# Optimization experiments

Measured on AMD Instinct MI355X. Metric: run time of the kernel, lower is better.

## Reference

```python
import jax, jax.numpy as jnp
import numpy as np

B, G, C = 8, 512, 32  # batch, grid size, channel width (INIT_DIM)
NPB = 32768           # nonzeros per batch element


def _sconv(x, k, stride, pad):
    # dense conv; sparse semantics recovered by masking with the output
    # coordinate occupancy (Minkowski conv only produces active outputs)
    return jax.lax.conv_general_dilated(
        x, k, (stride, stride), [(pad, pad), (pad, pad)],
        dimension_numbers=('NHWC', 'HWIO', 'NHWC'))


def _downsample_mask(m):
    # ME strided output coord exists iff any input coord in the 2x2 cell is active
    return jax.lax.reduce_window(m, 0.0, jax.lax.max, (1, 2, 2, 1), (1, 2, 2, 1), 'VALID')


def setup_inputs() -> dict:
    key = jax.random.key(0)
    ks = jax.random.split(key, 16)
    b = jnp.repeat(jnp.arange(B, dtype=jnp.int32), NPB)
    yx = jax.random.randint(ks[0], (B * NPB, 2), 0, G, dtype=jnp.int32)
    coords = jnp.concatenate([b[:, None], yx], axis=1)          # [N,3] (b,y,x)
    feats = jax.random.normal(ks[1], (B * NPB, 1), jnp.float32)  # 1 feature/nnz
    x2 = jax.random.normal(ks[2], (B, 3), jnp.float32)
    # Minkowski conv kernels (bias=False by default); HWIO layout
    K1 = jax.random.normal(ks[3], (5, 5, 1, C), jnp.float32) * 0.28   # kaiming-ish
    K2 = jax.random.normal(ks[4], (3, 3, C, C), jnp.float32) * 0.083
    K3 = jax.random.normal(ks[5], (3, 3, C, C), jnp.float32) * 0.083
    K4 = jax.random.normal(ks[6], (3, 3, C, C), jnp.float32) * 0.083
    # feature MLP: Linear(3,64) -> ReLU -> Linear(64,32)
    W1 = jax.random.normal(ks[7], (3, 64), jnp.float32) * 0.3
    b1 = jnp.zeros((64,), jnp.float32)
    W2 = jax.random.normal(ks[8], (64, 32), jnp.float32) * 0.25
    b2 = jnp.zeros((32,), jnp.float32)
    # matrix_embedding: Linear(64,128) -> ReLU
    W3 = jax.random.normal(ks[9], (64, 128), jnp.float32) * 0.18
    b3 = jnp.zeros((128,), jnp.float32)
    return {'coords': coords, 'feats': feats, 'x2': x2,
            'K1': K1, 'K2': K2, 'K3': K3, 'K4': K4,
            'W1': W1, 'b1': b1, 'W2': W2, 'b2': b2, 'W3': W3, 'b3': b3}


def reference(coords, feats, x2, K1, K2, K3, K4, W1, b1, W2, b2, W3, b3):
    bi, yi, xi = coords[:, 0], coords[:, 1], coords[:, 2]
    grid = jnp.zeros((B, G, G, 1), jnp.float32).at[bi, yi, xi, 0].set(feats[:, 0])
    m1 = jnp.zeros((B, G, G, 1), jnp.float32).at[bi, yi, xi, 0].set(1.0)
    # layer1: k=5 s=1 (output coords == input coords)
    y1 = jax.nn.relu(_sconv(grid, K1, 1, 2)) * m1
    # layers 2-4: k=3 s=2; centered at even positions, masked by strided occupancy
    m2 = _downsample_mask(m1)
    y2 = jax.nn.relu(_sconv(y1, K2, 2, 1)) * m2
    m3 = _downsample_mask(m2)
    y3 = jax.nn.relu(_sconv(y2, K3, 2, 1)) * m3
    m4 = _downsample_mask(m3)
    y4 = jax.nn.relu(_sconv(y3, K4, 2, 1)) * m4
    # global average pool over active output coordinates per batch
    cnt = jnp.sum(m4, axis=(1, 2))                      # [B,1]
    pooled = jnp.sum(y4, axis=(1, 2)) / jnp.maximum(cnt, 1.0)  # [B,32]
    # aux feature MLP
    h = jax.nn.relu(x2[:, :3] @ W1 + b1) @ W2 + b2      # [B,32]
    z = jnp.concatenate([pooled, h], axis=1)            # [B,64]
    return jax.nn.relu(z @ W3 + b3)                     # [B,128]
```

## Files before the change

### kernel.cpp

```cpp
#include <hip/hip_runtime.h>
#include <hip/hip_bf16.h>
#include <stdint.h>


static constexpr int G_ = 512;
static constexpr int NPTS = 8 * 32768;

#define DEVI __device__ __forceinline__

typedef __attribute__((ext_vector_type(8))) short bf16x8;
typedef __attribute__((ext_vector_type(4))) float f32x4;

DEVI float bf_lo(unsigned w) { return __uint_as_float(w << 16); }
DEVI float bf_hi(unsigned w) { return __uint_as_float(w & 0xFFFF0000u); }
DEVI unsigned comp(const uint4& v, int i) {
  return i == 0 ? v.x : i == 1 ? v.y : i == 2 ? v.z : v.w;
}
DEVI unsigned short f2bf_bits(float f) {
  unsigned u = __float_as_uint(f);
  unsigned r = u + 0x7FFFu + ((u >> 16) & 1u);
  return (unsigned short)(r >> 16);
}

__global__ __launch_bounds__(256) void k_scatter(const int* __restrict__ coords,
                                                 int* __restrict__ idxg) {
  int i = blockIdx.x * 256 + threadIdx.x;
  if (i >= NPTS) return;
  int b = coords[3 * i], y = coords[3 * i + 1], x = coords[3 * i + 2];
  atomicMax(&idxg[((size_t)b * G_ + y) * G_ + x], i);
}

__global__ __launch_bounds__(256) void k_grid(const int* __restrict__ idxg,
                                              const float* __restrict__ feats,
                                              float* __restrict__ grid) {
  int i = blockIdx.x * 256 + threadIdx.x;
  int v = idxg[i];
  grid[i] = (v >= 0) ? feats[v] : 0.0f;
}

__global__ __launch_bounds__(256) void k_m2(const int* __restrict__ idxg,
                                            float* __restrict__ m2) {
  int i = blockIdx.x * 256 + threadIdx.x;
  int b = i >> 16, r = (i >> 8) & 255, c = i & 255;
  const int* p = idxg + ((size_t)b * G_ + 2 * r) * G_ + 2 * c;
  bool occ = (p[0] >= 0) | (p[1] >= 0) | (p[G_] >= 0) | (p[G_ + 1] >= 0);
  m2[i] = occ ? 1.f : 0.f;
}

template <int WI>
__global__ __launch_bounds__(256) void k_pool_mask(const float* __restrict__ mi,
                                                   float* __restrict__ mo) {
  constexpr int WO = WI / 2;
  int i = blockIdx.x * 256 + threadIdx.x;
  int b = i / (WO * WO);
  int rem = i - b * WO * WO;
  int r = rem / WO, c = rem - r * WO;
  const float* p = mi + ((size_t)b * WI + 2 * r) * WI + 2 * c;
  mo[i] = fmaxf(fmaxf(p[0], p[1]), fmaxf(p[WI], p[WI + 1]));
}

__global__ __launch_bounds__(256) void k_conv1_mfma(
    const float* __restrict__ grid, const int* __restrict__ idxg,
    const float* __restrict__ K1f, __hip_bfloat16* __restrict__ y1) {
  constexpr int PITCH = 264;
  __shared__ unsigned short s_bh[2 * 64 * 8], s_bl[2 * 64 * 8];
  __shared__ float s_tile[8 * PITCH];

  const int t = threadIdx.x;
  const int b = blockIdx.z, R = blockIdx.y * 4, x0 = blockIdx.x * 256;

  for (int e = t; e < 128; e += 256) {
    int h = e >> 6, ln = e & 63;
    int g2 = ln >> 4, co = h * 16 + (ln & 15);
#pragma unroll
    for (int j = 0; j < 8; j++) {
      int k = 8 * g2 + j;
      float v = (k < 25) ? K1f[k * 32 + co] : 0.f;
      unsigned short hb = f2bf_bits(v);
      s_bh[e * 8 + j] = hb;
      s_bl[e * 8 + j] = f2bf_bits(v - __uint_as_float((unsigned)hb << 16));
    }
  }
  for (int i = t; i < 8 * 260; i += 256) {
    int rr = i / 260, cc = i - rr * 260;
    int gy = R - 2 + rr, gx = x0 - 2 + cc;
    float v = 0.f;
    if (gy >= 0 && gy < G_ && gx >= 0 && gx < G_)
      v = grid[((size_t)b * G_ + gy) * G_ + gx];
    s_tile[rr * PITCH + cc] = v;
  }
  __syncthreads();

  const int lane = t & 63, w = t >> 6;
  const int r = lane & 15, g = lane >> 4;
  bf16x8 bh[2], bl[2];
#pragma unroll
  for (int h = 0; h < 2; h++) {
    bh[h] = *(const bf16x8*)&s_bh[(h * 64 + lane) * 8];
    bl[h] = *(const bf16x8*)&s_bl[(h * 64 + lane) * 8];
  }
  int toff[8]; bool tval[8];
#pragma unroll
  for (int j = 0; j < 8; j++) {
    int k = 8 * g + j;
    tval[j] = (k < 25);
    int kq = tval[j] ? k : 0;
    int ky = kq / 5, kx = kq - 5 * ky;
    toff[j] = (w + ky) * PITCH + kx;
  }

  const int oy = R + w;
  const size_t rowo = ((size_t)b * G_ + oy) * G_;

  for (int s = 0; s < 16; s++) {
    const int oxl = s * 16;
    bf16x8 ahv, alv;
#pragma unroll
    for (int j = 0; j < 8; j++) {
      float v = tval[j] ? s_tile[toff[j] + oxl + r] : 0.f;
      unsigned short hb = f2bf_bits(v);
      ahv[j] = (short)hb;
      alv[j] = (short)f2bf_bits(v - __uint_as_float((unsigned)hb << 16));
    }
    f32x4 acc0 = {0.f, 0.f, 0.f, 0.f}, acc1 = {0.f, 0.f, 0.f, 0.f};
    acc0 = __builtin_amdgcn_mfma_f32_16x16x32_bf16(ahv, bh[0], acc0, 0, 0, 0);
    acc1 = __builtin_amdgcn_mfma_f32_16x16x32_bf16(ahv, bh[1], acc1, 0, 0, 0);
    acc0 = __builtin_amdgcn_mfma_f32_16x16x32_bf16(ahv, bl[0], acc0, 0, 0, 0);
    acc1 = __builtin_amdgcn_mfma_f32_16x16x32_bf16(ahv, bl[1], acc1, 0, 0, 0);
    acc0 = __builtin_amdgcn_mfma_f32_16x16x32_bf16(alv, bh[0], acc0, 0, 0, 0);
    acc1 = __builtin_amdgcn_mfma_f32_16x16x32_bf16(alv, bh[1], acc1, 0, 0, 0);

#pragma unroll
    for (int q = 0; q < 4; q++) {
      const size_t opix = rowo + (x0 + oxl + g * 4 + q);
      const float m = (idxg[opix] >= 0) ? 1.f : 0.f;
      unsigned short* op = (unsigned short*)(y1 + opix * 32);
      op[r] = f2bf_bits(fmaxf(acc0[q], 0.f) * m);
      op[r + 16] = f2bf_bits(fmaxf(acc1[q], 0.f) * m);
    }
  }
}

template <int HI, int SEGS>
__global__ __launch_bounds__(256) void k_conv3x3s2_mfma(
    const __hip_bfloat16* __restrict__ in, const float* __restrict__ Kw,
    const float* __restrict__ mask, __hip_bfloat16* __restrict__ out) {
  constexpr int WI = HI, HO = HI / 2, WO = WI / 2;
  constexpr int NSEG = WO / 16 / SEGS;
  __shared__ unsigned short s_pw[9 * 2 * 64 * 8];

  const int t = threadIdx.x;
  for (int e = t; e < 1152; e += 256) {
    int kk = e >> 7;
    int rem = e & 127;
    int h = rem >> 6, ln = rem & 63;
    int g = ln >> 4, co = h * 16 + (ln & 15);
#pragma unroll
    for (int j = 0; j < 8; j++)
      s_pw[e * 8 + j] = f2bf_bits(Kw[((kk * 32) + 8 * g + j) * 32 + co]);
  }
  __syncthreads();

  const int lane = t & 63, w = t >> 6;
  const int r = lane & 15, g = lane >> 4;
  bf16x8 bw[9][2];
#pragma unroll
  for (int kk = 0; kk < 9; kk++)
#pragma unroll
    for (int h = 0; h < 2; h++)
      bw[kk][h] = *(const bf16x8*)&s_pw[((kk * 2 + h) * 64 + lane) * 8];

  const int b = blockIdx.z;
  const int oy = blockIdx.y * 4 + w;
  const int ox_base = blockIdx.x * (WO / SEGS);
  const __hip_bfloat16* inb = in + (size_t)b * HI * WI * 32;

  for (int s = 0; s < NSEG; s++) {
    const int ox0 = ox_base + s * 16;
    f32x4 acc0 = {0.f, 0.f, 0.f, 0.f}, acc1 = {0.f, 0.f, 0.f, 0.f};
#pragma unroll
    for (int ky = 0; ky < 3; ky++) {
      const int iy = 2 * oy + ky - 1;
      const __hip_bfloat16* rowp = inb + (size_t)(iy < 0 ? 0 : iy) * WI * 32;
#pragma unroll
      for (int kx = 0; kx < 3; kx++) {
        const int ix = 2 * (ox0 + r) + kx - 1;
        uint4 v = *(const uint4*)(rowp + (size_t)(ix < 0 ? 0 : ix) * 32 + g * 8);
        if ((iy | ix) < 0) { v.x = 0; v.y = 0; v.z = 0; v.w = 0; }
        bf16x8 a = *reinterpret_cast<const bf16x8*>(&v);
        acc0 = __builtin_amdgcn_mfma_f32_16x16x32_bf16(a, bw[ky * 3 + kx][0],
                                                       acc0, 0, 0, 0);
        acc1 = __builtin_amdgcn_mfma_f32_16x16x32_bf16(a, bw[ky * 3 + kx][1],
                                                       acc1, 0, 0, 0);
      }
    }
    const size_t rowo = ((size_t)b * HO + oy) * WO;
#pragma unroll
    for (int q = 0; q < 4; q++) {
      const int rr = g * 4 + q;
      const size_t opix = rowo + (ox0 + rr);
      const float m = mask[opix];
      unsigned short* op = (unsigned short*)(out + opix * 32);
      op[r] = f2bf_bits(fmaxf(acc0[q], 0.f) * m);
      op[r + 16] = f2bf_bits(fmaxf(acc1[q], 0.f) * m);
    }
  }
}

__global__ __launch_bounds__(256) void k_pool(const __hip_bfloat16* __restrict__ y4,
                                              const float* __restrict__ m4,
                                              float* __restrict__ pooled) {
  const int b = blockIdx.x, t = threadIdx.x;
  const int c8 = t & 3, g = t >> 2;
  float s[8] = {0, 0, 0, 0, 0, 0, 0, 0};
  for (int p = g; p < 4096; p += 64) {
    uint4 raw = *(const uint4*)(y4 + ((size_t)b * 4096 + p) * 32 + c8 * 8);
#pragma unroll
    for (int cp = 0; cp < 4; cp++) {
      unsigned w = comp(raw, cp);
      s[2 * cp] += bf_lo(w);
      s[2 * cp + 1] += bf_hi(w);
    }
  }
  __shared__ float s_red[64][32];
  __shared__ float s_cnt[256];
#pragma unroll
  for (int j = 0; j < 8; j++) s_red[g][c8 * 8 + j] = s[j];
  float cnt = 0;
  for (int p = t; p < 4096; p += 256) cnt += m4[(size_t)b * 4096 + p];
  s_cnt[t] = cnt;
  __syncthreads();
  for (int st = 32; st > 0; st >>= 1) {
    if (g < st) {
#pragma unroll
      for (int j = 0; j < 8; j++) s_red[g][c8 * 8 + j] += s_red[g + st][c8 * 8 + j];
    }
    __syncthreads();
  }
  for (int st = 128; st > 0; st >>= 1) {
    if (t < st) s_cnt[t] += s_cnt[t + st];
    __syncthreads();
  }
  if (t < 32) pooled[b * 32 + t] = s_red[0][t] / fmaxf(s_cnt[0], 1.f);
}

__global__ __launch_bounds__(256) void k_mlp(
    const float* __restrict__ pooled, const float* __restrict__ x2,
    const float* __restrict__ W1, const float* __restrict__ b1,
    const float* __restrict__ W2, const float* __restrict__ b2,
    const float* __restrict__ W3, const float* __restrict__ b3,
    float* __restrict__ outp) {
  __shared__ float s_h1[8 * 64];
  __shared__ float s_z[8 * 64];
  const int t = threadIdx.x;
  for (int i = t; i < 512; i += 256) {
    int bb = i >> 6, j = i & 63;
    float a = b1[j] + x2[bb * 3 + 0] * W1[0 * 64 + j] +
              x2[bb * 3 + 1] * W1[1 * 64 + j] + x2[bb * 3 + 2] * W1[2 * 64 + j];
    s_h1[i] = fmaxf(a, 0.f);
  }
  __syncthreads();
  {
    int bb = t >> 5, ci = t & 31;
    float a = b2[ci];
    for (int k = 0; k < 64; k++) a += s_h1[bb * 64 + k] * W2[k * 32 + ci];
    s_z[bb * 64 + 32 + ci] = a;
    s_z[bb * 64 + ci] = pooled[bb * 32 + ci];
  }
  __syncthreads();
  for (int o = t; o < 1024; o += 256) {
    int bb = o >> 7, j = o & 127;
    float a = b3[j];
    for (int k = 0; k < 64; k++) a += s_z[bb * 64 + k] * W3[k * 128 + j];
    outp[o] = fmaxf(a, 0.f);
  }
}

extern "C" void kernel_launch(void* const* d_in, const int* in_sizes, int n_in,
                              void* d_out, int out_size, void* d_ws,
                              size_t ws_size, hipStream_t stream) {
  const int* coords = (const int*)d_in[0];
  const float* feats = (const float*)d_in[1];
  const float* x2 = (const float*)d_in[2];
  const float* K1 = (const float*)d_in[3];
  const float* K2 = (const float*)d_in[4];
  const float* K3 = (const float*)d_in[5];
  const float* K4 = (const float*)d_in[6];
  const float* W1 = (const float*)d_in[7];
  const float* b1 = (const float*)d_in[8];
  const float* W2 = (const float*)d_in[9];
  const float* b2 = (const float*)d_in[10];
  const float* W3 = (const float*)d_in[11];
  const float* b3 = (const float*)d_in[12];
  float* outp = (float*)d_out;

  char* ws = (char*)d_ws;
  size_t off = 0;
  auto alloc = [&](size_t bytes) {
    char* p = ws + off;
    off += (bytes + 255) & ~(size_t)255;
    return p;
  };
  int* idxg = (int*)alloc(8ull * 512 * 512 * 4);
  float* grid = (float*)alloc(8ull * 512 * 512 * 4);
  __hip_bfloat16* y1 = (__hip_bfloat16*)alloc(8ull * 512 * 512 * 32 * 2);
  __hip_bfloat16* y2 = (__hip_bfloat16*)alloc(8ull * 256 * 256 * 32 * 2);
  __hip_bfloat16* y3 = (__hip_bfloat16*)alloc(8ull * 128 * 128 * 32 * 2);
  __hip_bfloat16* y4 = (__hip_bfloat16*)alloc(8ull * 64 * 64 * 32 * 2);
  float* m2 = (float*)alloc(8ull * 256 * 256 * 4);
  float* m3 = (float*)alloc(8ull * 128 * 128 * 4);
  float* m4 = (float*)alloc(8ull * 64 * 64 * 4);
  float* pooled = (float*)alloc(8 * 32 * 4);
  (void)ws_size; (void)in_sizes; (void)n_in; (void)out_size;

  hipMemsetAsync(idxg, 0xFF, 8ull * 512 * 512 * 4, stream);

  k_scatter<<<NPTS / 256, 256, 0, stream>>>(coords, idxg);
  k_grid<<<(8 * 512 * 512) / 256, 256, 0, stream>>>(idxg, feats, grid);
  k_m2<<<(8 * 256 * 256) / 256, 256, 0, stream>>>(idxg, m2);
  k_pool_mask<256><<<(8 * 128 * 128) / 256, 256, 0, stream>>>(m2, m3);
  k_pool_mask<128><<<(8 * 64 * 64) / 256, 256, 0, stream>>>(m3, m4);

  k_conv1_mfma<<<dim3(2, 128, 8), 256, 0, stream>>>(grid, idxg, K1, y1);

  k_conv3x3s2_mfma<512, 2><<<dim3(2, 64, 8), 256, 0, stream>>>(y1, K2, m2, y2);
  k_conv3x3s2_mfma<256, 2><<<dim3(2, 32, 8), 256, 0, stream>>>(y2, K3, m3, y3);
  k_conv3x3s2_mfma<128, 2><<<dim3(2, 16, 8), 256, 0, stream>>>(y3, K4, m4, y4);

  k_pool<<<8, 256, 0, stream>>>(y4, m4, pooled);
  k_mlp<<<1, 256, 0, stream>>>(pooled, x2, W1, b1, W2, b2, W3, b3, outp);
}
```

Measured before the change: 246.1 us.

## Prepack weights and bf16 hi/lo grid once, fuse mask pyramid into one kernel

Adds a one-block kernel that converts all conv weights into MFMA fragment layout once, so conv blocks read prepacked bf16 fragments straight from global memory instead of each rebuilding them in shared memory. The grid kernel now stores the bf16 high/low split of each feature, so conv1 only repacks bits instead of converting per tap. The three mask kernels become one tiled kernel that builds m2, m3 and m4 through shared memory, removing two launches and the intermediate mask re-reads. The last stride-2 conv now uses single-wave blocks with more column segments, giving more blocks on a small layer at the cost of an extra small launch.

```diff
diff --git a/kernel.cpp b/kernel.cpp
--- a/kernel.cpp
+++ b/kernel.cpp
@@ -10,6 +10,7 @@
 
 typedef __attribute__((ext_vector_type(8))) short bf16x8;
 typedef __attribute__((ext_vector_type(4))) float f32x4;
+typedef __attribute__((ext_vector_type(4))) unsigned u32x4;
 
 DEVI float bf_lo(unsigned w) { return __uint_as_float(w << 16); }
 DEVI float bf_hi(unsigned w) { return __uint_as_float(w & 0xFFFF0000u); }
@@ -32,72 +33,104 @@
 
 __global__ __launch_bounds__(256) void k_grid(const int* __restrict__ idxg,
                                               const float* __restrict__ feats,
-                                              float* __restrict__ grid) {
+                                              unsigned* __restrict__ grid2) {
   int i = blockIdx.x * 256 + threadIdx.x;
   int v = idxg[i];
-  grid[i] = (v >= 0) ? feats[v] : 0.0f;
-}
-
-__global__ __launch_bounds__(256) void k_m2(const int* __restrict__ idxg,
-                                            float* __restrict__ m2) {
-  int i = blockIdx.x * 256 + threadIdx.x;
-  int b = i >> 16, r = (i >> 8) & 255, c = i & 255;
-  const int* p = idxg + ((size_t)b * G_ + 2 * r) * G_ + 2 * c;
-  bool occ = (p[0] >= 0) | (p[1] >= 0) | (p[G_] >= 0) | (p[G_ + 1] >= 0);
-  m2[i] = occ ? 1.f : 0.f;
-}
-
-template <int WI>
-__global__ __launch_bounds__(256) void k_pool_mask(const float* __restrict__ mi,
-                                                   float* __restrict__ mo) {
-  constexpr int WO = WI / 2;
-  int i = blockIdx.x * 256 + threadIdx.x;
-  int b = i / (WO * WO);
-  int rem = i - b * WO * WO;
-  int r = rem / WO, c = rem - r * WO;
-  const float* p = mi + ((size_t)b * WI + 2 * r) * WI + 2 * c;
-  mo[i] = fmaxf(fmaxf(p[0], p[1]), fmaxf(p[WI], p[WI + 1]));
-}
-
-__global__ __launch_bounds__(256) void k_conv1_mfma(
-    const float* __restrict__ grid, const int* __restrict__ idxg,
-    const float* __restrict__ K1f, __hip_bfloat16* __restrict__ y1) {
-  constexpr int PITCH = 264;
-  __shared__ unsigned short s_bh[2 * 64 * 8], s_bl[2 * 64 * 8];
-  __shared__ float s_tile[8 * PITCH];
-
-  const int t = threadIdx.x;
-  const int b = blockIdx.z, R = blockIdx.y * 4, x0 = blockIdx.x * 256;
-
-  for (int e = t; e < 128; e += 256) {
-    int h = e >> 6, ln = e & 63;
+  float f = (v >= 0) ? feats[v] : 0.0f;
+  unsigned short hb = f2bf_bits(f);
+  unsigned short lb = f2bf_bits(f - __uint_as_float((unsigned)hb << 16));
+  grid2[i] = (unsigned)hb | ((unsigned)lb << 16);
+}
+
+__global__ __launch_bounds__(256) void k_packw(
+    const float* __restrict__ K1f, const float* __restrict__ K2,
+    const float* __restrict__ K3, const float* __restrict__ K4,
+    unsigned short* __restrict__ pw1h, unsigned short* __restrict__ pw1l,
+    unsigned short* __restrict__ pw2, unsigned short* __restrict__ pw3,
+    unsigned short* __restrict__ pw4) {
+  const int t = threadIdx.x;
+  if (t < 128) {
+    int h = t >> 6, ln = t & 63;
     int g2 = ln >> 4, co = h * 16 + (ln & 15);
 #pragma unroll
     for (int j = 0; j < 8; j++) {
       int k = 8 * g2 + j;
       float v = (k < 25) ? K1f[k * 32 + co] : 0.f;
       unsigned short hb = f2bf_bits(v);
-      s_bh[e * 8 + j] = hb;
-      s_bl[e * 8 + j] = f2bf_bits(v - __uint_as_float((unsigned)hb << 16));
-    }
-  }
+      pw1h[t * 8 + j] = hb;
+      pw1l[t * 8 + j] = f2bf_bits(v - __uint_as_float((unsigned)hb << 16));
+    }
+  }
+  const float* Ks[3] = {K2, K3, K4};
+  unsigned short* ps[3] = {pw2, pw3, pw4};
+  for (int m = 0; m < 3; m++)
+    for (int e = t; e < 1152; e += 256) {
+      int kk = e >> 7, rem = e & 127;
+      int h = rem >> 6, ln = rem & 63;
+      int g2 = ln >> 4, co = h * 16 + (ln & 15);
+#pragma unroll
+      for (int j = 0; j < 8; j++)
+        ps[m][e * 8 + j] = f2bf_bits(Ks[m][((kk * 32) + 8 * g2 + j) * 32 + co]);
+    }
+}
+
+__global__ __launch_bounds__(256) void k_masks(const int* __restrict__ idxg,
+                                               float* __restrict__ m2,
+                                               float* __restrict__ m3,
+                                               float* __restrict__ m4) {
+  __shared__ float sm2[32][32];
+  __shared__ float sm3[16][16];
+  const int b = blockIdx.z, ty0 = blockIdx.y * 32, tx0 = blockIdx.x * 32;
+  const int t = threadIdx.x;
+  for (int i = t; i < 1024; i += 256) {
+    int r = i >> 5, c = i & 31;
+    const int* p = idxg + ((size_t)b * 512 + 2 * (ty0 + r)) * 512 + 2 * (tx0 + c);
+    float v = ((p[0] & p[1] & p[512] & p[513]) >= 0) ? 1.f : 0.f;
+    m2[((size_t)b * 256 + ty0 + r) * 256 + tx0 + c] = v;
+    sm2[r][c] = v;
+  }
+  __syncthreads();
+  {
+    int r = t >> 4, c = t & 15;
+    float v = fmaxf(fmaxf(sm2[2 * r][2 * c], sm2[2 * r][2 * c + 1]),
+                    fmaxf(sm2[2 * r + 1][2 * c], sm2[2 * r + 1][2 * c + 1]));
+    m3[((size_t)b * 128 + (ty0 >> 1) + r) * 128 + (tx0 >> 1) + c] = v;
+    sm3[r][c] = v;
+  }
+  __syncthreads();
+  if (t < 64) {
+    int r = t >> 3, c = t & 7;
+    float v = fmaxf(fmaxf(sm3[2 * r][2 * c], sm3[2 * r][2 * c + 1]),
+                    fmaxf(sm3[2 * r + 1][2 * c], sm3[2 * r + 1][2 * c + 1]));
+    m4[((size_t)b * 64 + (ty0 >> 2) + r) * 64 + (tx0 >> 2) + c] = v;
+  }
+}
+
+__global__ __launch_bounds__(256) void k_conv1_mfma(
+    const unsigned* __restrict__ grid2, const int* __restrict__ idxg,
+    const unsigned short* __restrict__ pw1h,
+    const unsigned short* __restrict__ pw1l,
+    __hip_bfloat16* __restrict__ y1) {
+  constexpr int PITCH = 264;
+  __shared__ unsigned s_tile[8 * PITCH];
+  const int t = threadIdx.x;
+  const int b = blockIdx.z, R = blockIdx.y * 4, x0 = blockIdx.x * 256;
   for (int i = t; i < 8 * 260; i += 256) {
     int rr = i / 260, cc = i - rr * 260;
     int gy = R - 2 + rr, gx = x0 - 2 + cc;
-    float v = 0.f;
+    unsigned v = 0;
     if (gy >= 0 && gy < G_ && gx >= 0 && gx < G_)
-      v = grid[((size_t)b * G_ + gy) * G_ + gx];
+      v = grid2[((size_t)b * G_ + gy) * G_ + gx];
     s_tile[rr * PITCH + cc] = v;
   }
-  __syncthreads();
 
   const int lane = t & 63, w = t >> 6;
   const int r = lane & 15, g = lane >> 4;
   bf16x8 bh[2], bl[2];
 #pragma unroll
   for (int h = 0; h < 2; h++) {
-    bh[h] = *(const bf16x8*)&s_bh[(h * 64 + lane) * 8];
-    bl[h] = *(const bf16x8*)&s_bl[(h * 64 + lane) * 8];
+    bh[h] = *(const bf16x8*)&pw1h[(h * 64 + lane) * 8];
+    bl[h] = *(const bf16x8*)&pw1l[(h * 64 + lane) * 8];
   }
   int toff[8]; bool tval[8];
 #pragma unroll
@@ -108,20 +141,26 @@
     int ky = kq / 5, kx = kq - 5 * ky;
     toff[j] = (w + ky) * PITCH + kx;
   }
+  __syncthreads();
 
   const int oy = R + w;
   const size_t rowo = ((size_t)b * G_ + oy) * G_;
 
   for (int s = 0; s < 16; s++) {
     const int oxl = s * 16;
-    bf16x8 ahv, alv;
-#pragma unroll
-    for (int j = 0; j < 8; j++) {
-      float v = tval[j] ? s_tile[toff[j] + oxl + r] : 0.f;
-      unsigned short hb = f2bf_bits(v);
-      ahv[j] = (short)hb;
-      alv[j] = (short)f2bf_bits(v - __uint_as_float((unsigned)hb << 16));
-    }
+    unsigned wv[8];
+#pragma unroll
+    for (int j = 0; j < 8; j++)
+      wv[j] = tval[j] ? s_tile[toff[j] + oxl + r] : 0u;
+    u32x4 ua, ul;
+#pragma unroll
+    for (int p = 0; p < 4; p++) {
+      unsigned w0 = wv[2 * p], w1 = wv[2 * p + 1];
+      ua[p] = (w0 & 0xffffu) | (w1 << 16);
+      ul[p] = (w0 >> 16) | (w1 & 0xffff0000u);
+    }
+    bf16x8 ahv = __builtin_bit_cast(bf16x8, ua);
+    bf16x8 alv = __builtin_bit_cast(bf16x8, ul);
     f32x4 acc0 = {0.f, 0.f, 0.f, 0.f}, acc1 = {0.f, 0.f, 0.f, 0.f};
     acc0 = __builtin_amdgcn_mfma_f32_16x16x32_bf16(ahv, bh[0], acc0, 0, 0, 0);
     acc1 = __builtin_amdgcn_mfma_f32_16x16x32_bf16(ahv, bh[1], acc1, 0, 0, 0);
@@ -141,26 +180,14 @@
   }
 }
 
-template <int HI, int SEGS>
-__global__ __launch_bounds__(256) void k_conv3x3s2_mfma(
-    const __hip_bfloat16* __restrict__ in, const float* __restrict__ Kw,
+template <int HI, int SEGS, int NW>
+__global__ __launch_bounds__(NW * 64) void k_conv3x3s2_mfma(
+    const __hip_bfloat16* __restrict__ in,
+    const unsigned short* __restrict__ pw,
     const float* __restrict__ mask, __hip_bfloat16* __restrict__ out) {
   constexpr int WI = HI, HO = HI / 2, WO = WI / 2;
   constexpr int NSEG = WO / 16 / SEGS;
-  __shared__ unsigned short s_pw[9 * 2 * 64 * 8];
-
-  const int t = threadIdx.x;
-  for (int e = t; e < 1152; e += 256) {
-    int kk = e >> 7;
-    int rem = e & 127;
-    int h = rem >> 6, ln = rem & 63;
-    int g = ln >> 4, co = h * 16 + (ln & 15);
-#pragma unroll
-    for (int j = 0; j < 8; j++)
-      s_pw[e * 8 + j] = f2bf_bits(Kw[((kk * 32) + 8 * g + j) * 32 + co]);
-  }
-  __syncthreads();
-
+  const int t = threadIdx.x;
   const int lane = t & 63, w = t >> 6;
   const int r = lane & 15, g = lane >> 4;
   bf16x8 bw[9][2];
@@ -168,10 +195,10 @@
   for (int kk = 0; kk < 9; kk++)
 #pragma unroll
     for (int h = 0; h < 2; h++)
-      bw[kk][h] = *(const bf16x8*)&s_pw[((kk * 2 + h) * 64 + lane) * 8];
+      bw[kk][h] = *(const bf16x8*)&pw[((kk * 2 + h) * 64 + lane) * 8];
 
   const int b = blockIdx.z;
-  const int oy = blockIdx.y * 4 + w;
+  const int oy = blockIdx.y * NW + w;
   const int ox_base = blockIdx.x * (WO / SEGS);
   const __hip_bfloat16* inb = in + (size_t)b * HI * WI * 32;
 
@@ -197,8 +224,7 @@
     const size_t rowo = ((size_t)b * HO + oy) * WO;
 #pragma unroll
     for (int q = 0; q < 4; q++) {
-      const int rr = g * 4 + q;
-      const size_t opix = rowo + (ox0 + rr);
+      const size_t opix = rowo + (ox0 + g * 4 + q);
       const float m = mask[opix];
       unsigned short* op = (unsigned short*)(out + opix * 32);
       op[r] = f2bf_bits(fmaxf(acc0[q], 0.f) * m);
@@ -302,7 +328,7 @@
     return p;
   };
   int* idxg = (int*)alloc(8ull * 512 * 512 * 4);
-  float* grid = (float*)alloc(8ull * 512 * 512 * 4);
+  unsigned* grid2 = (unsigned*)alloc(8ull * 512 * 512 * 4);
   __hip_bfloat16* y1 = (__hip_bfloat16*)alloc(8ull * 512 * 512 * 32 * 2);
   __hip_bfloat16* y2 = (__hip_bfloat16*)alloc(8ull * 256 * 256 * 32 * 2);
   __hip_bfloat16* y3 = (__hip_bfloat16*)alloc(8ull * 128 * 128 * 32 * 2);
@@ -311,21 +337,25 @@
   float* m3 = (float*)alloc(8ull * 128 * 128 * 4);
   float* m4 = (float*)alloc(8ull * 64 * 64 * 4);
   float* pooled = (float*)alloc(8 * 32 * 4);
+  unsigned short* pw1h = (unsigned short*)alloc(128 * 8 * 2);
+  unsigned short* pw1l = (unsigned short*)alloc(128 * 8 * 2);
+  unsigned short* pw2 = (unsigned short*)alloc(1152 * 8 * 2);
+  unsigned short* pw3 = (unsigned short*)alloc(1152 * 8 * 2);
+  unsigned short* pw4 = (unsigned short*)alloc(1152 * 8 * 2);
   (void)ws_size; (void)in_sizes; (void)n_in; (void)out_size;
 
   hipMemsetAsync(idxg, 0xFF, 8ull * 512 * 512 * 4, stream);
 
+  k_packw<<<1, 256, 0, stream>>>(K1, K2, K3, K4, pw1h, pw1l, pw2, pw3, pw4);
   k_scatter<<<NPTS / 256, 256, 0, stream>>>(coords, idxg);
-  k_grid<<<(8 * 512 * 512) / 256, 256, 0, stream>>>(idxg, feats, grid);
-  k_m2<<<(8 * 256 * 256) / 256, 256, 0, stream>>>(idxg, m2);
-  k_pool_mask<256><<<(8 * 128 * 128) / 256, 256, 0, stream>>>(m2, m3);
-  k_pool_mask<128><<<(8 * 64 * 64) / 256, 256, 0, stream>>>(m3, m4);
-
-  k_conv1_mfma<<<dim3(2, 128, 8), 256, 0, stream>>>(grid, idxg, K1, y1);
-
-  k_conv3x3s2_mfma<512, 2><<<dim3(2, 64, 8), 256, 0, stream>>>(y1, K2, m2, y2);
-  k_conv3x3s2_mfma<256, 2><<<dim3(2, 32, 8), 256, 0, stream>>>(y2, K3, m3, y3);
-  k_conv3x3s2_mfma<128, 2><<<dim3(2, 16, 8), 256, 0, stream>>>(y3, K4, m4, y4);
+  k_grid<<<(8 * 512 * 512) / 256, 256, 0, stream>>>(idxg, feats, grid2);
+  k_masks<<<dim3(8, 8, 8), 256, 0, stream>>>(idxg, m2, m3, m4);
+
+  k_conv1_mfma<<<dim3(2, 128, 8), 256, 0, stream>>>(grid2, idxg, pw1h, pw1l, y1);
+
+  k_conv3x3s2_mfma<512, 2, 4><<<dim3(2, 64, 8), 256, 0, stream>>>(y1, pw2, m2, y2);
+  k_conv3x3s2_mfma<256, 2, 4><<<dim3(2, 32, 8), 256, 0, stream>>>(y2, pw3, m3, y3);
+  k_conv3x3s2_mfma<128, 4, 1><<<dim3(4, 64, 8), 64, 0, stream>>>(y3, pw4, m4, y4);
 
   k_pool<<<8, 256, 0, stream>>>(y4, m4, pooled);
   k_mlp<<<1, 256, 0, stream>>>(pooled, x2, W1, b1, W2, b2, W3, b3, outp);
```

Result: faster. 237.1 us (-3.7%).
